# Kernel tuning notes

Hardware: AMD Instinct MI355X
Metric: run time of the kernel (lower is better)

Reference implementation:

```python
import jax, jax.numpy as jnp
import numpy as np
from jax import lax

# 4th-order Butterworth lowpass, scipy.signal.butter(4, 0.2)
B_COEF = np.array([0.004824343357716228, 0.019297373430864913, 0.02894606014629737,
                   0.019297373430864913, 0.004824343357716228], dtype=np.float32)
A_COEF = np.array([1.0, -2.369513007182038, 2.3139884144006453,
                   -1.0546654058785672, 0.18737949236818502], dtype=np.float32)


def setup_inputs() -> dict:
    key = jax.random.key(0)
    x = jax.random.normal(key, (8, 64, 48000), dtype=jnp.float32)
    return {"x": x, "b": jnp.asarray(B_COEF), "a": jnp.asarray(A_COEF)}


def _pad_odd(x, n):
    # Faithful to torch _pad_odd (including its exact slicing on the right side).
    left = 2.0 * x[..., 0:1] - jnp.flip(x[..., 0:n], axis=-1)
    right = 2.0 * x[..., -1:] - jnp.flip(x[..., -(n + 2):-2], axis=-1)
    return jnp.concatenate([left, x, right], axis=-1)


def _lfilter(x, a, b):
    # y[n] = (sum_k b[k] x[n-k] - sum_j a[j] y[n-j]) / a[0]
    a0 = a[0]
    bn = b / a0
    an = a[1:] / a0                      # [N], N = order
    ntaps = b.shape[0]                   # static
    N = a.shape[0] - 1                   # static
    T = x.shape[-1]
    # FIR part: small static tap loop, fully vectorized over batch/time.
    pad = [(0, 0)] * (x.ndim - 1) + [(ntaps - 1, 0)]
    xp = jnp.pad(x, pad)
    f = bn[0] * xp[..., ntaps - 1: ntaps - 1 + T]
    for k in range(1, ntaps):
        f = f + bn[k] * xp[..., ntaps - 1 - k: ntaps - 1 - k + T]
    # IIR recurrence via scan over time.
    f_t = jnp.moveaxis(f, -1, 0)         # [T, B, C]
    init = jnp.zeros(x.shape[:-1] + (N,), x.dtype)  # [B, C, N], y[t-1..t-N]

    def step(carry, ft):
        y = ft - jnp.einsum('k,...k->...', an, carry)
        carry = jnp.concatenate([y[..., None], carry[..., :-1]], axis=-1)
        return carry, y

    _, ys = lax.scan(step, init, f_t)
    return jnp.moveaxis(ys, 0, -1)       # [B, C, T]


def _filtfilt(x, a, b):
    y = _lfilter(x, a, b)
    return jnp.flip(_lfilter(jnp.flip(y, axis=-1), a, b), axis=-1)


def reference(x, b, a):
    scale = jnp.max(jnp.abs(x), axis=-1, keepdims=True)
    xs = x / scale
    padlen = 3 * max(int(a.shape[0]), int(b.shape[0]))  # 15, static
    xp = _pad_odd(xs, padlen)
    y = _filtfilt(xp, a, b)
    y = y[..., padlen:-padlen]
    return y * scale
```

## Files before the change

### kernel.cpp

```cpp
#include <hip/hip_runtime.h>


#define T48 48000
#define TP0 48030
#define LCH 24
#define UPB 504

#define BAR_LDS() do { \
  asm volatile("s_waitcnt lgkmcnt(0)" ::: "memory"); \
  __builtin_amdgcn_s_barrier(); \
} while (0)

__device__ __forceinline__ float fget(const float4& v, int e) {
  switch (e & 3) { case 0: return v.x; case 1: return v.y; case 2: return v.z; default: return v.w; }
}

#define MAPPLY(t, M, q) do { \
  (t).x += (M)[0]*(q).x  + (M)[1]*(q).y  + (M)[2]*(q).z  + (M)[3]*(q).w; \
  (t).y += (M)[4]*(q).x  + (M)[5]*(q).y  + (M)[6]*(q).z  + (M)[7]*(q).w; \
  (t).z += (M)[8]*(q).x  + (M)[9]*(q).y  + (M)[10]*(q).z + (M)[11]*(q).w; \
  (t).w += (M)[12]*(q).x + (M)[13]*(q).y + (M)[14]*(q).z + (M)[15]*(q).w; \
} while (0)

__global__ __launch_bounds__(512, 4) void filtfilt_k(
    const float* __restrict__ x, const float* __restrict__ bco,
    const float* __restrict__ aco, float* __restrict__ out)
{
  __shared__ __align__(16) float4 S[2048];
  __shared__ float P[3][16];

  const int t   = threadIdx.x;
  const int seq = blockIdx.x >> 2;
  const int b   = blockIdx.x & 3;
  const int gc  = UPB*b - 4 + t;
  const float* __restrict__ xs = x + (size_t)seq * T48;
  const float4* __restrict__ xs4 = reinterpret_cast<const float4*>(xs);
  float* __restrict__ os = out + (size_t)seq * T48;
  float4* __restrict__ os4 = reinterpret_cast<float4*>(os);

  const float inva0 = 1.f / aco[0];
  const float b0 = bco[0]*inva0, b1 = bco[1]*inva0, b2 = bco[2]*inva0,
              b3 = bco[3]*inva0, b4 = bco[4]*inva0;
  const float na1 = -aco[1]*inva0, na2 = -aco[2]*inva0,
              na3 = -aco[3]*inva0, na4 = -aco[4]*inva0;

  float4 F[8];
  const int fb = 6*gc - 5;
#pragma unroll
  for (int k = 0; k < 8; k++) {
    int m = min(max(fb + k, 0), 11999);
    F[k] = xs4[m];
  }

  if (t < 64) {
    const int i = (t >> 2) & 3, j = t & 3;
    float r1 = (j==0)?1.f:0.f, r2 = (j==1)?1.f:0.f,
          r3 = (j==2)?1.f:0.f, r4 = (j==3)?1.f:0.f;
#pragma unroll
    for (int n = 0; n < LCH; n++) {
      float h = fmaf(na1, r1, fmaf(na2, r2, fmaf(na3, r3, na4 * r4)));
      r4 = r3; r3 = r2; r2 = r1; r1 = h;
    }
    float c0 = __shfl(r1, j), c1 = __shfl(r2, j),
          c2 = __shfl(r3, j), c3 = __shfl(r4, j);
    float Pv = (i==0)?c0 : (i==1)?c1 : (i==2)?c2 : c3;
    if (t < 16) P[0][t] = Pv;
    const float P0v = Pv;
    {
      float rA0 = __shfl(Pv, i*4+0), rA1 = __shfl(Pv, i*4+1),
            rA2 = __shfl(Pv, i*4+2), rA3 = __shfl(Pv, i*4+3);
      float cB0 = __shfl(Pv, 0*4+j), cB1 = __shfl(Pv, 1*4+j),
            cB2 = __shfl(Pv, 2*4+j), cB3 = __shfl(Pv, 3*4+j);
      Pv = rA0*cB0 + rA1*cB1 + rA2*cB2 + rA3*cB3;
    }
    if (t < 16) P[1][t] = Pv;
    {
      float rA0 = __shfl(Pv, i*4+0), rA1 = __shfl(Pv, i*4+1),
            rA2 = __shfl(Pv, i*4+2), rA3 = __shfl(Pv, i*4+3);
      float cB0 = __shfl(P0v, 0*4+j), cB1 = __shfl(P0v, 1*4+j),
            cB2 = __shfl(P0v, 2*4+j), cB3 = __shfl(P0v, 3*4+j);
      Pv = rA0*cB0 + rA1*cB1 + rA2*cB2 + rA3*cB3;
    }
    if (t < 16) P[2][t] = Pv;
  }

  float w4v = F[0].y, w3v = F[0].z, w2v = F[0].w, w1v = F[1].x;
  float A[LCH];
#pragma unroll
  for (int n = 0; n < LCH; n++) A[n] = fget(F[(n + 5) >> 2], (n + 5) & 3);

  if (gc < 0) {
    w4v = 0.f; w3v = 0.f; w2v = 0.f; w1v = 0.f;
#pragma unroll
    for (int n = 0; n < LCH; n++) A[n] = 0.f;
  } else if (gc == 0) {
    float x0d = 2.f * xs[0];
    w4v = 0.f; w3v = 0.f; w2v = 0.f; w1v = 0.f;
#pragma unroll
    for (int n = 0; n < 15; n++) A[n] = x0d - xs[14 - n];
  }
  if (gc >= 2000) {
    float xld = 2.f * xs[T48 - 1];
#define RFIX(p, var) do { int _p = (p); \
    if (_p >= 48015) var = (_p < TP0) ? (xld - xs[96012 - _p]) : 0.f; } while (0)
    RFIX(24*gc - 4, w4v); RFIX(24*gc - 3, w3v);
    RFIX(24*gc - 2, w2v); RFIX(24*gc - 1, w1v);
#pragma unroll
    for (int n = 0; n < LCH; n++) {
      int p = 24*gc + n;
      if (p >= 48015) A[n] = (p < TP0) ? (xld - xs[96012 - p]) : 0.f;
    }
#undef RFIX
  }

  float r1 = 0.f, r2 = 0.f, r3 = 0.f, r4 = 0.f;
#pragma unroll
  for (int n = 0; n < LCH; n++) {
    float xv = A[n];
    float f = fmaf(b0,xv, fmaf(b1,w1v, fmaf(b2,w2v, fmaf(b3,w3v, b4*w4v))));
    w4v = w3v; w3v = w2v; w2v = w1v; w1v = xv;
    float u = fmaf(na4, r4, f);
    u = fmaf(na3, r3, u); u = fmaf(na2, r2, u); u = fmaf(na1, r1, u);
    A[n] = u; r4 = r3; r3 = r2; r2 = r1; r1 = u;
  }

  S[t] = make_float4(r1, r2, r3, r4);
  BAR_LDS();
  float4 sv = make_float4(0.f,0.f,0.f,0.f);
  if (t >= 1) sv = S[t-1];
  if (t >= 2) { float4 q = S[t-2]; MAPPLY(sv, P[0], q); }
  if (t >= 3) { float4 q = S[t-3]; MAPPLY(sv, P[1], q); }
  if (t >= 4) { float4 q = S[t-4]; MAPPLY(sv, P[2], q); }

  {
    float h1 = sv.x, h2 = sv.y, h3 = sv.z, h4 = sv.w;
#pragma unroll
    for (int n = 0; n < LCH; n++) {
      float h = fmaf(na1, h1, fmaf(na2, h2, fmaf(na3, h3, na4 * h4)));
      A[n] += h;
      h4 = h3; h3 = h2; h2 = h1; h1 = h;
    }
  }
  if (gc >= 2000) {
#pragma unroll
    for (int n = 0; n < LCH; n++) if (24*gc + n >= TP0) A[n] = 0.f;
  }

  S[512 + t] = make_float4(A[0], A[1], A[2], A[3]);
  BAR_LDS();
  float h0 = 0.f, h1v = 0.f, h2v = 0.f, h3v = 0.f;
  if (t < 511) { float4 hv = S[512 + t + 1]; h0 = hv.x; h1v = hv.y; h2v = hv.z; h3v = hv.w; }

#define YV(i) ((i) < 24 ? A[(i)] : ((i)==24 ? h0 : (i)==25 ? h1v : (i)==26 ? h2v : h3v))
  r1 = 0.f; r2 = 0.f; r3 = 0.f; r4 = 0.f;
#pragma unroll
  for (int m = 0; m < LCH; m++) {
    float g = fmaf(b0, YV(23-m), fmaf(b1, YV(24-m),
              fmaf(b2, YV(25-m), fmaf(b3, YV(26-m), b4 * YV(27-m)))));
    float u = fmaf(na4, r4, g);
    u = fmaf(na3, r3, u); u = fmaf(na2, r2, u); u = fmaf(na1, r1, u);
    r4 = r3; r3 = r2; r2 = r1; r1 = u;
    if      (m == 0) h3v = u;
    else if (m == 1) h2v = u;
    else if (m == 2) h1v = u;
    else if (m == 3) h0  = u;
    else             A[27 - m] = u;
  }
#undef YV

  S[1024 + t] = make_float4(r1, r2, r3, r4);
  BAR_LDS();
  float4 ev = make_float4(0.f,0.f,0.f,0.f);
  if (t <= 510) ev = S[1024 + t + 1];
  if (t <= 509) { float4 q = S[1024 + t + 2]; MAPPLY(ev, P[0], q); }
  if (t <= 508) { float4 q = S[1024 + t + 3]; MAPPLY(ev, P[1], q); }
  if (t <= 507) { float4 q = S[1024 + t + 4]; MAPPLY(ev, P[2], q); }
  BAR_LDS();

  {
    float g1 = ev.x, g2 = ev.y, g3 = ev.z, g4 = ev.w;
#pragma unroll
    for (int m = 0; m < LCH; m++) {
      float h = fmaf(na1, g1, fmaf(na2, g2, fmaf(na3, g3, na4 * g4)));
      if      (m == 0) h3v += h;
      else if (m == 1) h2v += h;
      else if (m == 2) h1v += h;
      else if (m == 3) h0  += h;
      else             A[27 - m] += h;
      g4 = g3; g3 = g2; g2 = g1; g1 = h;
    }
  }

  S[t]        = make_float4(A[4],  A[5],  A[6],  A[7]);
  S[512 + t]  = make_float4(A[8],  A[9],  A[10], A[11]);
  S[1024 + t] = make_float4(A[12], A[13], A[14], A[15]);
  S[1536 + t] = make_float4(A[16], A[17], A[18], A[19]);
  BAR_LDS();
  if (t >= 4 && t < 508 && gc <= 1999) {
    float4 N0 = S[t+1], N1 = S[512 + t+1], N2 = S[1024 + t+1], N3 = S[1536 + t+1];
    float4* op = os4 + 6*gc;
    op[0] = make_float4(A[19], A[20], A[21], A[22]);
    op[1] = make_float4(A[23], h0,    h1v,   h2v);
    op[2] = make_float4(h3v,   N0.x,  N0.y,  N0.z);
    op[3] = make_float4(N0.w,  N1.x,  N1.y,  N1.z);
    op[4] = make_float4(N1.w,  N2.x,  N2.y,  N2.z);
    op[5] = make_float4(N2.w,  N3.x,  N3.y,  N3.z);
  }
}

extern "C" void kernel_launch(void* const* d_in, const int* in_sizes, int n_in,
                              void* d_out, int out_size, void* d_ws, size_t ws_size,
                              hipStream_t stream) {
  (void)n_in; (void)d_ws; (void)ws_size; (void)out_size;
  const float* x = (const float*)d_in[0];
  const float* b = (const float*)d_in[1];
  const float* a = (const float*)d_in[2];
  float* out = (float*)d_out;
  const int nseq = in_sizes[0] / T48;
  filtfilt_k<<<dim3(nseq * 4), dim3(512), 0, stream>>>(x, b, a, out);
}
```

Before: 202.7 us.

## Process two sequences per block and prefetch the second input during the first

Each block now handles two sequences one after the other, reusing the propagation matrices P it computes once. The global loads for the second sequence's input are issued in two halves partway through the first sequence's compute, so load latency overlaps with arithmetic. The grid is halved, which cuts the redundant per-block P setup. In exchange it adds eight float4 prefetch registers, which may raise register pressure under the 512x4 launch bounds, and leaves fewer blocks to hide latency.

```diff
diff --git a/kernel.cpp b/kernel.cpp
--- a/kernel.cpp
+++ b/kernel.cpp
@@ -22,6 +22,158 @@
   (t).w += (M)[12]*(q).x + (M)[13]*(q).y + (M)[14]*(q).z + (M)[15]*(q).w; \
 } while (0)
 
+struct Cf { float b0,b1,b2,b3,b4, na1,na2,na3,na4; };
+
+template<bool PRE>
+__device__ __forceinline__ void pass_pipeline(
+    const int t, const int gc, const float4* __restrict__ F,
+    const float* __restrict__ xs, float4* __restrict__ os4,
+    const float (* __restrict__ P)[16], float4* __restrict__ S, const Cf cf,
+    const float4* __restrict__ xn4, const int fbn, float4* __restrict__ FB)
+{
+  const float b0 = cf.b0, b1 = cf.b1, b2 = cf.b2, b3 = cf.b3, b4 = cf.b4;
+  const float na1 = cf.na1, na2 = cf.na2, na3 = cf.na3, na4 = cf.na4;
+
+  float w4v = F[0].y, w3v = F[0].z, w2v = F[0].w, w1v = F[1].x;
+  float A[LCH];
+#pragma unroll
+  for (int n = 0; n < LCH; n++) A[n] = fget(F[(n + 5) >> 2], (n + 5) & 3);
+
+  if (gc < 0) {
+    w4v = 0.f; w3v = 0.f; w2v = 0.f; w1v = 0.f;
+#pragma unroll
+    for (int n = 0; n < LCH; n++) A[n] = 0.f;
+  } else if (gc == 0) {
+    float x0d = 2.f * xs[0];
+    w4v = 0.f; w3v = 0.f; w2v = 0.f; w1v = 0.f;
+#pragma unroll
+    for (int n = 0; n < 15; n++) A[n] = x0d - xs[14 - n];
+  }
+  if (gc >= 2000) {
+    float xld = 2.f * xs[T48 - 1];
+#define RFIX(p, var) do { int _p = (p); \
+    if (_p >= 48015) var = (_p < TP0) ? (xld - xs[96012 - _p]) : 0.f; } while (0)
+    RFIX(24*gc - 4, w4v); RFIX(24*gc - 3, w3v);
+    RFIX(24*gc - 2, w2v); RFIX(24*gc - 1, w1v);
+#pragma unroll
+    for (int n = 0; n < LCH; n++) {
+      int p = 24*gc + n;
+      if (p >= 48015) A[n] = (p < TP0) ? (xld - xs[96012 - p]) : 0.f;
+    }
+#undef RFIX
+  }
+
+  if constexpr (PRE) {
+#pragma unroll
+    for (int k = 0; k < 4; k++) {
+      int m = min(max(fbn + k, 0), 11999);
+      FB[k] = xn4[m];
+    }
+  }
+
+  float r1 = 0.f, r2 = 0.f, r3 = 0.f, r4 = 0.f;
+#pragma unroll
+  for (int n = 0; n < LCH; n++) {
+    float xv = A[n];
+    float f = fmaf(b0,xv, fmaf(b1,w1v, fmaf(b2,w2v, fmaf(b3,w3v, b4*w4v))));
+    w4v = w3v; w3v = w2v; w2v = w1v; w1v = xv;
+    float u = fmaf(na4, r4, f);
+    u = fmaf(na3, r3, u); u = fmaf(na2, r2, u); u = fmaf(na1, r1, u);
+    A[n] = u; r4 = r3; r3 = r2; r2 = r1; r1 = u;
+  }
+
+  S[t] = make_float4(r1, r2, r3, r4);
+  BAR_LDS();
+  float4 sv = make_float4(0.f,0.f,0.f,0.f);
+  if (t >= 1) sv = S[t-1];
+  if (t >= 2) { float4 q = S[t-2]; MAPPLY(sv, P[0], q); }
+  if (t >= 3) { float4 q = S[t-3]; MAPPLY(sv, P[1], q); }
+  if (t >= 4) { float4 q = S[t-4]; MAPPLY(sv, P[2], q); }
+
+  {
+    float h1 = sv.x, h2 = sv.y, h3 = sv.z, h4 = sv.w;
+#pragma unroll
+    for (int n = 0; n < LCH; n++) {
+      float h = fmaf(na1, h1, fmaf(na2, h2, fmaf(na3, h3, na4 * h4)));
+      A[n] += h;
+      h4 = h3; h3 = h2; h2 = h1; h1 = h;
+    }
+  }
+  if (gc >= 2000) {
+#pragma unroll
+    for (int n = 0; n < LCH; n++) if (24*gc + n >= TP0) A[n] = 0.f;
+  }
+
+  S[512 + t] = make_float4(A[0], A[1], A[2], A[3]);
+  BAR_LDS();
+  float h0 = 0.f, h1v = 0.f, h2v = 0.f, h3v = 0.f;
+  if (t < 511) { float4 hv = S[512 + t + 1]; h0 = hv.x; h1v = hv.y; h2v = hv.z; h3v = hv.w; }
+
+#define YV(i) ((i) < 24 ? A[(i)] : ((i)==24 ? h0 : (i)==25 ? h1v : (i)==26 ? h2v : h3v))
+  r1 = 0.f; r2 = 0.f; r3 = 0.f; r4 = 0.f;
+#pragma unroll
+  for (int m = 0; m < LCH; m++) {
+    float g = fmaf(b0, YV(23-m), fmaf(b1, YV(24-m),
+              fmaf(b2, YV(25-m), fmaf(b3, YV(26-m), b4 * YV(27-m)))));
+    float u = fmaf(na4, r4, g);
+    u = fmaf(na3, r3, u); u = fmaf(na2, r2, u); u = fmaf(na1, r1, u);
+    r4 = r3; r3 = r2; r2 = r1; r1 = u;
+    if      (m == 0) h3v = u;
+    else if (m == 1) h2v = u;
+    else if (m == 2) h1v = u;
+    else if (m == 3) h0  = u;
+    else             A[27 - m] = u;
+  }
+#undef YV
+
+  if constexpr (PRE) {
+#pragma unroll
+    for (int k = 4; k < 8; k++) {
+      int m = min(max(fbn + k, 0), 11999);
+      FB[k] = xn4[m];
+    }
+  }
+
+  S[1024 + t] = make_float4(r1, r2, r3, r4);
+  BAR_LDS();
+  float4 ev = make_float4(0.f,0.f,0.f,0.f);
+  if (t <= 510) ev = S[1024 + t + 1];
+  if (t <= 509) { float4 q = S[1024 + t + 2]; MAPPLY(ev, P[0], q); }
+  if (t <= 508) { float4 q = S[1024 + t + 3]; MAPPLY(ev, P[1], q); }
+  if (t <= 507) { float4 q = S[1024 + t + 4]; MAPPLY(ev, P[2], q); }
+  BAR_LDS();
+
+  {
+    float g1 = ev.x, g2 = ev.y, g3 = ev.z, g4 = ev.w;
+#pragma unroll
+    for (int m = 0; m < LCH; m++) {
+      float h = fmaf(na1, g1, fmaf(na2, g2, fmaf(na3, g3, na4 * g4)));
+      if      (m == 0) h3v += h;
+      else if (m == 1) h2v += h;
+      else if (m == 2) h1v += h;
+      else if (m == 3) h0  += h;
+      else             A[27 - m] += h;
+      g4 = g3; g3 = g2; g2 = g1; g1 = h;
+    }
+  }
+
+  S[t]        = make_float4(A[4],  A[5],  A[6],  A[7]);
+  S[512 + t]  = make_float4(A[8],  A[9],  A[10], A[11]);
+  S[1024 + t] = make_float4(A[12], A[13], A[14], A[15]);
+  S[1536 + t] = make_float4(A[16], A[17], A[18], A[19]);
+  BAR_LDS();
+  if (t >= 4 && t < 508 && gc <= 1999) {
+    float4 N0 = S[t+1], N1 = S[512 + t+1], N2 = S[1024 + t+1], N3 = S[1536 + t+1];
+    float4* op = os4 + 6*gc;
+    op[0] = make_float4(A[19], A[20], A[21], A[22]);
+    op[1] = make_float4(A[23], h0,    h1v,   h2v);
+    op[2] = make_float4(h3v,   N0.x,  N0.y,  N0.z);
+    op[3] = make_float4(N0.w,  N1.x,  N1.y,  N1.z);
+    op[4] = make_float4(N1.w,  N2.x,  N2.y,  N2.z);
+    op[5] = make_float4(N2.w,  N3.x,  N3.y,  N3.z);
+  }
+}
+
 __global__ __launch_bounds__(512, 4) void filtfilt_k(
     const float* __restrict__ x, const float* __restrict__ bco,
     const float* __restrict__ aco, float* __restrict__ out)
@@ -29,27 +181,27 @@
   __shared__ __align__(16) float4 S[2048];
   __shared__ float P[3][16];
 
-  const int t   = threadIdx.x;
-  const int seq = blockIdx.x >> 2;
-  const int b   = blockIdx.x & 3;
-  const int gc  = UPB*b - 4 + t;
-  const float* __restrict__ xs = x + (size_t)seq * T48;
-  const float4* __restrict__ xs4 = reinterpret_cast<const float4*>(xs);
-  float* __restrict__ os = out + (size_t)seq * T48;
-  float4* __restrict__ os4 = reinterpret_cast<float4*>(os);
+  const int t    = threadIdx.x;
+  const int pair = blockIdx.x >> 2;
+  const int b    = blockIdx.x & 3;
+  const int gc   = UPB*b - 4 + t;
+  const float* __restrict__ xsA = x + (size_t)(2*pair)     * T48;
+  const float* __restrict__ xsB = x + (size_t)(2*pair + 1) * T48;
+  const float4* __restrict__ xsA4 = reinterpret_cast<const float4*>(xsA);
+  const float4* __restrict__ xsB4 = reinterpret_cast<const float4*>(xsB);
+  float4* __restrict__ osA4 = reinterpret_cast<float4*>(out + (size_t)(2*pair)     * T48);
+  float4* __restrict__ osB4 = reinterpret_cast<float4*>(out + (size_t)(2*pair + 1) * T48);
 
   const float inva0 = 1.f / aco[0];
-  const float b0 = bco[0]*inva0, b1 = bco[1]*inva0, b2 = bco[2]*inva0,
-              b3 = bco[3]*inva0, b4 = bco[4]*inva0;
-  const float na1 = -aco[1]*inva0, na2 = -aco[2]*inva0,
-              na3 = -aco[3]*inva0, na4 = -aco[4]*inva0;
-
-  float4 F[8];
+  const Cf cf = { bco[0]*inva0, bco[1]*inva0, bco[2]*inva0, bco[3]*inva0, bco[4]*inva0,
+                  -aco[1]*inva0, -aco[2]*inva0, -aco[3]*inva0, -aco[4]*inva0 };
+
+  float4 FA[8];
   const int fb = 6*gc - 5;
 #pragma unroll
   for (int k = 0; k < 8; k++) {
     int m = min(max(fb + k, 0), 11999);
-    F[k] = xs4[m];
+    FA[k] = xsA4[m];
   }
 
   if (t < 64) {
@@ -58,7 +210,7 @@
           r3 = (j==2)?1.f:0.f, r4 = (j==3)?1.f:0.f;
 #pragma unroll
     for (int n = 0; n < LCH; n++) {
-      float h = fmaf(na1, r1, fmaf(na2, r2, fmaf(na3, r3, na4 * r4)));
+      float h = fmaf(cf.na1, r1, fmaf(cf.na2, r2, fmaf(cf.na3, r3, cf.na4 * r4)));
       r4 = r3; r3 = r2; r2 = r1; r1 = h;
     }
     float c0 = __shfl(r1, j), c1 = __shfl(r2, j),
@@ -84,128 +236,12 @@
     if (t < 16) P[2][t] = Pv;
   }
 
-  float w4v = F[0].y, w3v = F[0].z, w2v = F[0].w, w1v = F[1].x;
-  float A[LCH];
-#pragma unroll
-  for (int n = 0; n < LCH; n++) A[n] = fget(F[(n + 5) >> 2], (n + 5) & 3);
-
-  if (gc < 0) {
-    w4v = 0.f; w3v = 0.f; w2v = 0.f; w1v = 0.f;
-#pragma unroll
-    for (int n = 0; n < LCH; n++) A[n] = 0.f;
-  } else if (gc == 0) {
-    float x0d = 2.f * xs[0];
-    w4v = 0.f; w3v = 0.f; w2v = 0.f; w1v = 0.f;
-#pragma unroll
-    for (int n = 0; n < 15; n++) A[n] = x0d - xs[14 - n];
-  }
-  if (gc >= 2000) {
-    float xld = 2.f * xs[T48 - 1];
-#define RFIX(p, var) do { int _p = (p); \
-    if (_p >= 48015) var = (_p < TP0) ? (xld - xs[96012 - _p]) : 0.f; } while (0)
-    RFIX(24*gc - 4, w4v); RFIX(24*gc - 3, w3v);
-    RFIX(24*gc - 2, w2v); RFIX(24*gc - 1, w1v);
-#pragma unroll
-    for (int n = 0; n < LCH; n++) {
-      int p = 24*gc + n;
-      if (p >= 48015) A[n] = (p < TP0) ? (xld - xs[96012 - p]) : 0.f;
-    }
-#undef RFIX
-  }
-
-  float r1 = 0.f, r2 = 0.f, r3 = 0.f, r4 = 0.f;
-#pragma unroll
-  for (int n = 0; n < LCH; n++) {
-    float xv = A[n];
-    float f = fmaf(b0,xv, fmaf(b1,w1v, fmaf(b2,w2v, fmaf(b3,w3v, b4*w4v))));
-    w4v = w3v; w3v = w2v; w2v = w1v; w1v = xv;
-    float u = fmaf(na4, r4, f);
-    u = fmaf(na3, r3, u); u = fmaf(na2, r2, u); u = fmaf(na1, r1, u);
-    A[n] = u; r4 = r3; r3 = r2; r2 = r1; r1 = u;
-  }
-
-  S[t] = make_float4(r1, r2, r3, r4);
-  BAR_LDS();
-  float4 sv = make_float4(0.f,0.f,0.f,0.f);
-  if (t >= 1) sv = S[t-1];
-  if (t >= 2) { float4 q = S[t-2]; MAPPLY(sv, P[0], q); }
-  if (t >= 3) { float4 q = S[t-3]; MAPPLY(sv, P[1], q); }
-  if (t >= 4) { float4 q = S[t-4]; MAPPLY(sv, P[2], q); }
-
-  {
-    float h1 = sv.x, h2 = sv.y, h3 = sv.z, h4 = sv.w;
-#pragma unroll
-    for (int n = 0; n < LCH; n++) {
-      float h = fmaf(na1, h1, fmaf(na2, h2, fmaf(na3, h3, na4 * h4)));
-      A[n] += h;
-      h4 = h3; h3 = h2; h2 = h1; h1 = h;
-    }
-  }
-  if (gc >= 2000) {
-#pragma unroll
-    for (int n = 0; n < LCH; n++) if (24*gc + n >= TP0) A[n] = 0.f;
-  }
-
-  S[512 + t] = make_float4(A[0], A[1], A[2], A[3]);
-  BAR_LDS();
-  float h0 = 0.f, h1v = 0.f, h2v = 0.f, h3v = 0.f;
-  if (t < 511) { float4 hv = S[512 + t + 1]; h0 = hv.x; h1v = hv.y; h2v = hv.z; h3v = hv.w; }
-
-#define YV(i) ((i) < 24 ? A[(i)] : ((i)==24 ? h0 : (i)==25 ? h1v : (i)==26 ? h2v : h3v))
-  r1 = 0.f; r2 = 0.f; r3 = 0.f; r4 = 0.f;
-#pragma unroll
-  for (int m = 0; m < LCH; m++) {
-    float g = fmaf(b0, YV(23-m), fmaf(b1, YV(24-m),
-              fmaf(b2, YV(25-m), fmaf(b3, YV(26-m), b4 * YV(27-m)))));
-    float u = fmaf(na4, r4, g);
-    u = fmaf(na3, r3, u); u = fmaf(na2, r2, u); u = fmaf(na1, r1, u);
-    r4 = r3; r3 = r2; r2 = r1; r1 = u;
-    if      (m == 0) h3v = u;
-    else if (m == 1) h2v = u;
-    else if (m == 2) h1v = u;
-    else if (m == 3) h0  = u;
-    else             A[27 - m] = u;
-  }
-#undef YV
-
-  S[1024 + t] = make_float4(r1, r2, r3, r4);
-  BAR_LDS();
-  float4 ev = make_float4(0.f,0.f,0.f,0.f);
-  if (t <= 510) ev = S[1024 + t + 1];
-  if (t <= 509) { float4 q = S[1024 + t + 2]; MAPPLY(ev, P[0], q); }
-  if (t <= 508) { float4 q = S[1024 + t + 3]; MAPPLY(ev, P[1], q); }
-  if (t <= 507) { float4 q = S[1024 + t + 4]; MAPPLY(ev, P[2], q); }
-  BAR_LDS();
-
-  {
-    float g1 = ev.x, g2 = ev.y, g3 = ev.z, g4 = ev.w;
-#pragma unroll
-    for (int m = 0; m < LCH; m++) {
-      float h = fmaf(na1, g1, fmaf(na2, g2, fmaf(na3, g3, na4 * g4)));
-      if      (m == 0) h3v += h;
-      else if (m == 1) h2v += h;
-      else if (m == 2) h1v += h;
-      else if (m == 3) h0  += h;
-      else             A[27 - m] += h;
-      g4 = g3; g3 = g2; g2 = g1; g1 = h;
-    }
-  }
-
-  S[t]        = make_float4(A[4],  A[5],  A[6],  A[7]);
-  S[512 + t]  = make_float4(A[8],  A[9],  A[10], A[11]);
-  S[1024 + t] = make_float4(A[12], A[13], A[14], A[15]);
-  S[1536 + t] = make_float4(A[16], A[17], A[18], A[19]);
-  BAR_LDS();
-  if (t >= 4 && t < 508 && gc <= 1999) {
-    float4 N0 = S[t+1], N1 = S[512 + t+1], N2 = S[1024 + t+1], N3 = S[1536 + t+1];
-    float4* op = os4 + 6*gc;
-    op[0] = make_float4(A[19], A[20], A[21], A[22]);
-    op[1] = make_float4(A[23], h0,    h1v,   h2v);
-    op[2] = make_float4(h3v,   N0.x,  N0.y,  N0.z);
-    op[3] = make_float4(N0.w,  N1.x,  N1.y,  N1.z);
-    op[4] = make_float4(N1.w,  N2.x,  N2.y,  N2.z);
-    op[5] = make_float4(N2.w,  N3.x,  N3.y,  N3.z);
-  }
+  float4 FB[8];
+  pass_pipeline<true >(t, gc, FA, xsA, osA4, P, S, cf, xsB4, fb, FB);
+
+  BAR_LDS();
+
+  pass_pipeline<false>(t, gc, FB, xsB, osB4, P, S, cf, xsB4, fb, FB);
 }
 
 extern "C" void kernel_launch(void* const* d_in, const int* in_sizes, int n_in,
@@ -217,5 +253,5 @@
   const float* a = (const float*)d_in[2];
   float* out = (float*)d_out;
   const int nseq = in_sizes[0] / T48;
-  filtfilt_k<<<dim3(nseq * 4), dim3(512), 0, stream>>>(x, b, a, out);
-}
+  filtfilt_k<<<dim3((nseq / 2) * 4), dim3(512), 0, stream>>>(x, b, a, out);
+}
```

Result: no change. 205.3 us (+1.3%).
